# Optimization experiments

Hardware: AMD Instinct MI355X
Metric: run time of the kernel (lower is better)

Reference implementation:

```python
import jax, jax.numpy as jnp
import numpy as np

GRID = 4
N = GRID * GRID  # 16 nodes
CIN = 16
HID = 64
HEADS = 4
OUT = 256
NEG_SLOPE = 0.2  # PyG GATConv default leaky relu slope
LN_EPS = 1e-5


def _adj_mask():
    # 4-connected grid adjacency + self loops (PyG GATConv add_self_loops=True)
    m = np.zeros((N, N), dtype=bool)
    for i in range(GRID):
        for j in range(GRID):
            u = i * GRID + j
            if j + 1 < GRID:
                v = i * GRID + j + 1
                m[u, v] = m[v, u] = True
            if i + 1 < GRID:
                v = (i + 1) * GRID + j
                m[u, v] = m[v, u] = True
    np.fill_diagonal(m, True)
    return m

ADJ = jnp.asarray(_adj_mask())  # [N, N], adj[i, j] = j is a (self-)neighbor of i


def gat_layer(h, W, a_src, a_dst, b, concat):
    """PyG GATConv on the fixed grid graph, dense-masked form.
    h: [B, N, Fin]; W: [Fin, HEADS*C]; a_src/a_dst: [HEADS, C]."""
    B = h.shape[0]
    H, C = a_src.shape
    wh = (h @ W).reshape(B, N, H, C)                       # [B, N, H, C]
    e_src = jnp.einsum('bnhc,hc->bnh', wh, a_src)          # alpha_src . Wh_j
    e_dst = jnp.einsum('bnhc,hc->bnh', wh, a_dst)          # alpha_dst . Wh_i
    # score[b, i, j, h]: target i attends to source j
    e = e_dst[:, :, None, :] + e_src[:, None, :, :]
    e = jax.nn.leaky_relu(e, NEG_SLOPE)
    e = jnp.where(ADJ[None, :, :, None], e, -1e9)
    alpha = jax.nn.softmax(e, axis=2)                      # softmax over sources j
    out = jnp.einsum('bijh,bjhc->bihc', alpha, wh)         # [B, N, H, C]
    if concat:
        out = out.reshape(B, N, H * C)
    else:
        out = out.mean(axis=2)
    return out + b


def setup_inputs() -> dict:
    key = jax.random.key(0)
    ks = jax.random.split(key, 24)
    s = 0.05
    B = 16384
    inp = {
        'x': jax.random.normal(ks[0], (B, CIN, GRID, GRID), dtype=jnp.float32),
        'w_in': jax.random.normal(ks[1], (CIN, HID), dtype=jnp.float32) * s,
        'b_in': jnp.zeros((HID,), jnp.float32),
        # GAT layer 0: in 64 -> 4 heads x 64, concat
        'W0': jax.random.normal(ks[2], (HID, HEADS * HID), dtype=jnp.float32) * s,
        'asrc0': jax.random.normal(ks[3], (HEADS, HID), dtype=jnp.float32) * s,
        'adst0': jax.random.normal(ks[4], (HEADS, HID), dtype=jnp.float32) * s,
        'bb0': jnp.zeros((HEADS * HID,), jnp.float32),
        # GAT layer 1: in 256 -> 4 heads x 64, concat
        'W1': jax.random.normal(ks[5], (HEADS * HID, HEADS * HID), dtype=jnp.float32) * s,
        'asrc1': jax.random.normal(ks[6], (HEADS, HID), dtype=jnp.float32) * s,
        'adst1': jax.random.normal(ks[7], (HEADS, HID), dtype=jnp.float32) * s,
        'bb1': jnp.zeros((HEADS * HID,), jnp.float32),
        # GAT layer 2: in 256 -> 4 heads x 64, mean over heads (concat=False)
        'W2': jax.random.normal(ks[8], (HEADS * HID, HEADS * HID), dtype=jnp.float32) * s,
        'asrc2': jax.random.normal(ks[9], (HEADS, HID), dtype=jnp.float32) * s,
        'adst2': jax.random.normal(ks[10], (HEADS, HID), dtype=jnp.float32) * s,
        'bb2': jnp.zeros((HID,), jnp.float32),
        # output MLP: 64 -> 128 (LN, ReLU) -> 256
        'w1': jax.random.normal(ks[11], (HID, OUT // 2), dtype=jnp.float32) * s,
        'b1': jnp.zeros((OUT // 2,), jnp.float32),
        'ln_g': jnp.ones((OUT // 2,), jnp.float32),
        'ln_b': jnp.zeros((OUT // 2,), jnp.float32),
        'w2': jax.random.normal(ks[12], (OUT // 2, OUT), dtype=jnp.float32) * s,
        'b2': jnp.zeros((OUT,), jnp.float32),
    }
    return inp


def reference(x, w_in, b_in, W0, asrc0, adst0, bb0, W1, asrc1, adst1, bb1,
              W2, asrc2, adst2, bb2, w1, b1, ln_g, ln_b, w2, b2):
    B = x.shape[0]
    # grid_to_graph: (B, C, H, W) -> (B, N, C) node features
    h = jnp.transpose(x, (0, 2, 3, 1)).reshape(B, N, CIN)
    h = jax.nn.relu(h @ w_in + b_in)
    h = gat_layer(h, W0, asrc0, adst0, bb0, concat=True)
    h = jax.nn.relu(h)  # dropout is identity at inference
    h = gat_layer(h, W1, asrc1, adst1, bb1, concat=True)
    h = jax.nn.relu(h)
    h = gat_layer(h, W2, asrc2, adst2, bb2, concat=False)  # [B, N, 64]
    g = h.mean(axis=1)  # global_mean_pool over the 16 nodes of each graph
    # MLP with LayerNorm
    y = g @ w1 + b1
    mu = y.mean(axis=-1, keepdims=True)
    var = ((y - mu) ** 2).mean(axis=-1, keepdims=True)
    y = (y - mu) * jax.lax.rsqrt(var + LN_EPS) * ln_g + ln_b
    y = jax.nn.relu(y)
    return y @ w2 + b2
```

## Files before the change

### kernel.cpp

```cpp
#include <hip/hip_runtime.h>
#include <hip/hip_bf16.h>

typedef short s8v __attribute__((ext_vector_type(8)));
typedef short s4v __attribute__((ext_vector_type(4)));
typedef float f4v __attribute__((ext_vector_type(4)));

#define WSTR 36
#define AP   20
#define HIXBASE(s, quad) (((s)*4 + (quad))*256)

__device__ constexpr unsigned KMASK[16] = {
  0x0013u,0x0027u,0x004Eu,0x008Cu,
  0x0131u,0x0272u,0x04E4u,0x08C8u,
  0x1310u,0x2720u,0x4E40u,0x8C80u,
  0x3100u,0x7200u,0xE400u,0xC800u};

__device__ __forceinline__ short f2b(float x){
  __hip_bfloat16 h = __float2bfloat16(x);
  return *reinterpret_cast<short*>(&h);
}
__device__ __forceinline__ float b2f(short s){
  __hip_bfloat16 h = *reinterpret_cast<__hip_bfloat16*>(&s);
  return __bfloat162float(h);
}
__device__ __forceinline__ unsigned pk2(float a, float b){
  unsigned ua = __float_as_uint(a), ub = __float_as_uint(b);
  ua += 0x7fffu + ((ua >> 16) & 1u);
  ub += 0x7fffu + ((ub >> 16) & 1u);
  return __builtin_amdgcn_perm(ub, ua, 0x07060302);
}

__global__ __launch_bounds__(256) void prep_all(
  const float* __restrict__ W0, const float* __restrict__ as0, const float* __restrict__ ad0,
  const float* __restrict__ W1, const float* __restrict__ as1, const float* __restrict__ ad1,
  const float* __restrict__ W2, const float* __restrict__ as2, const float* __restrict__ ad2,
  const float* __restrict__ w_in,
  short* __restrict__ ws)
{
  short* WPin = ws;
  short* WP0  = ws + 2048;
  short* WP1  = ws + 2048 + 17408;
  short* WP2  = ws + 2048 + 17408 + 69632;

  const int t = threadIdx.x, l = t & 63;
  const int gid = blockIdx.x*4 + (t >> 6);

  if (gid < 288){
    const float* W; short* WP; int u = gid, f, s, KS;
    if (u < 32)      { W = W0; WP = WP0; KS = 2; f = u >> 1; s = u & 1; }
    else if (u < 160){ u -= 32;  W = W1; WP = WP1; KS = 8; f = u >> 3; s = u & 7; }
    else             { u -= 160; W = W2; WP = WP2; KS = 8; f = u >> 3; s = u & 7; }
    const int lq = l & 15, quad = l >> 4;
    union { s8v v; short s16[8]; } o;
    #pragma unroll
    for (int j = 0; j < 8; ++j)
      o.s16[j] = f2b(W[(s*32 + quad*8 + j)*256 + f*16 + lq]);
    *(s8v*)(WP + ((f*KS + s)*64 + l)*8) = o.v;
  } else if (gid < 292){
    const int f = gid - 288;
    const int lq = l & 15, quad = l >> 4;
    union { s8v v; short s16[8]; } o;
    #pragma unroll
    for (int j = 0; j < 8; ++j){
      const int k = quad*8 + j;
      o.s16[j] = (k < 16) ? f2b(w_in[k*64 + f*16 + lq]) : (short)0;
    }
    *(s8v*)(WPin + (f*64 + l)*8) = o.v;
  } else {
    int u = gid - 292;
    const float* W; const float* as; const float* ad; short* WP; int KS, k;
    if (u < 64)      { W=W0; as=as0; ad=ad0; WP=WP0; KS=2; k=u; }
    else if (u < 320){ u-=64;  W=W1; as=as1; ad=ad1; WP=WP1; KS=8; k=u; }
    else             { u-=320; W=W2; as=as2; ad=ad2; WP=WP2; KS=8; k=u; }
    float v[8];
    #pragma unroll
    for (int h = 0; h < 4; ++h){
      const float wv_ = W[k*256 + h*64 + l];
      v[h]   = wv_ * as[h*64 + l];
      v[4+h] = wv_ * ad[h*64 + l];
    }
    #pragma unroll
    for (int s = 1; s < 64; s <<= 1)
      #pragma unroll
      for (int uu = 0; uu < 8; ++uu) v[uu] += __shfl_xor(v[uu], s, 64);
    if (l < 16){
      const float r = (l < 8) ? v[l] : 0.f;
      WP[((16*KS + (k >> 5))*64 + ((k >> 3) & 3)*16 + l)*8 + (k & 7)] = f2b(r);
    }
  }
}

template<int KS, bool MEAN>
__device__ __forceinline__ void gat_layer(short* bufH, short* whT, short* alphaS,
    const short* __restrict__ WP, const float* __restrict__ bbias,
    float* __restrict__ out, const int b, const int t)
{
  const int l = t & 63, wv = t >> 6, lq = l & 15, quad = l >> 4;
  {
    f4v acc[5][2];
    #pragma unroll
    for (int fi = 0; fi < 5; ++fi)
      #pragma unroll
      for (int nt = 0; nt < 2; ++nt) acc[fi][nt] = (f4v){0.f,0.f,0.f,0.f};
    #pragma unroll
    for (int s = 0; s < KS; ++s){
      const s8v a0 = *(const s8v*)&bufH[HIXBASE(s, quad) + lq*8];
      const s8v a1 = *(const s8v*)&bufH[HIXBASE(s, quad) + (16 + lq)*8];
      #pragma unroll
      for (int fi = 0; fi < 5; ++fi){
        if (fi == 4 && wv != 3) break;
        const int f = (fi == 4) ? 16 : fi*4 + wv;
        const s8v bF = *(const s8v*)&WP[((f*KS + s)*64 + l)*8];
        acc[fi][0] = __builtin_amdgcn_mfma_f32_16x16x32_bf16(a0, bF, acc[fi][0], 0,0,0);
        acc[fi][1] = __builtin_amdgcn_mfma_f32_16x16x32_bf16(a1, bF, acc[fi][1], 0,0,0);
      }
    }
    #pragma unroll
    for (int fi = 0; fi < 5; ++fi){
      if (fi == 4 && (wv != 3 || lq >= 8)) break;
      const int f = (fi == 4) ? 16 : fi*4 + wv;
      #pragma unroll
      for (int nt = 0; nt < 2; ++nt){
        uint2 p;
        p.x = pk2(acc[fi][nt][0], acc[fi][nt][1]);
        p.y = pk2(acc[fi][nt][2], acc[fi][nt][3]);
        *(uint2*)&whT[(f*16 + lq)*WSTR + nt*16 + quad*4] = p;
      }
    }
  }
  __syncthreads();
  if (t < 128){
    const int g = t >> 6, h = (t >> 4) & 3, i = t & 15;
    const float ed = b2f(whT[(260 + h)*WSTR + g*16 + i]);
    float ev[16];
    #pragma unroll
    for (int c = 0; c < 4; ++c){
      const s4v v = *(const s4v*)&whT[(256 + h)*WSTR + g*16 + c*4];
      ev[c*4+0]=b2f(v[0]); ev[c*4+1]=b2f(v[1]); ev[c*4+2]=b2f(v[2]); ev[c*4+3]=b2f(v[3]);
    }
    const unsigned m = KMASK[i];
    float ssum = 0.f;
    #pragma unroll
    for (int j = 0; j < 16; ++j){
      float e = ed + ev[j];
      e = (e > 0.f) ? e : 0.2f*e;
      const float a = ((m >> j) & 1u) ? __expf(e) : 0.f;
      ev[j] = a; ssum += a;
    }
    const float inv = 1.f / ssum;
    unsigned* row = (unsigned*)&alphaS[((g*4 + h)*16 + i)*AP];
    #pragma unroll
    for (int c = 0; c < 8; ++c)
      row[c] = pk2(ev[2*c]*inv, ev[2*c+1]*inv);
  }
  __syncthreads();
  if constexpr (!MEAN){
    const int h = wv;
    union { s8v v; unsigned u[4]; } B[2];
    #pragma unroll
    for (int g = 0; g < 2; ++g){
      const unsigned* ar = (const unsigned*)&alphaS[((g*4 + h)*16 + lq)*AP + (quad & 1)*8];
      const bool act = ((quad >> 1) == g);
      #pragma unroll
      for (int c = 0; c < 4; ++c) B[g].u[c] = act ? ar[c] : 0u;
    }
    #pragma unroll
    for (int ct = 0; ct < 4; ++ct){
      const s8v a = *(const s8v*)&whT[(h*64 + ct*16 + lq)*WSTR + quad*8];
      const int sf = h*2 + (ct >> 1);
      const int qf = (ct & 1)*2 + (quad >> 1);
      const int jf = (quad & 1)*4;
      const int f0 = h*64 + ct*16 + quad*4;
      const float4 bb = *(const float4*)&bbias[f0];
      #pragma unroll
      for (int g = 0; g < 2; ++g){
        f4v d = (f4v){0.f,0.f,0.f,0.f};
        d = __builtin_amdgcn_mfma_f32_16x16x32_bf16(a, B[g].v, d, 0,0,0);
        uint2 p;
        p.x = pk2(fmaxf(d[0] + bb.x, 0.f), fmaxf(d[1] + bb.y, 0.f));
        p.y = pk2(fmaxf(d[2] + bb.z, 0.f), fmaxf(d[3] + bb.w, 0.f));
        *(uint2*)&bufH[HIXBASE(sf, qf) + (g*16 + lq)*8 + jf] = p;
      }
    }
  } else {
    const int g = wv >> 1;
    union { s8v v; unsigned u[4]; } B[4];
    #pragma unroll
    for (int h = 0; h < 4; ++h){
      const unsigned* ar = (const unsigned*)&alphaS[((g*4 + h)*16 + lq)*AP + (quad & 1)*8];
      const bool act = ((quad >> 1) == g);
      #pragma unroll
      for (int c = 0; c < 4; ++c) B[h].u[c] = act ? ar[c] : 0u;
    }
    #pragma unroll
    for (int cc = 0; cc < 2; ++cc){
      const int ct = (wv & 1)*2 + cc;
      f4v d = (f4v){0.f,0.f,0.f,0.f};
      #pragma unroll
      for (int h = 0; h < 4; ++h){
        const s8v a = *(const s8v*)&whT[(h*64 + ct*16 + lq)*WSTR + quad*8];
        d = __builtin_amdgcn_mfma_f32_16x16x32_bf16(a, B[h].v, d, 0,0,0);
      }
      #pragma unroll
      for (int s = 1; s < 16; s <<= 1){
        d[0] += __shfl_xor(d[0], s, 64); d[1] += __shfl_xor(d[1], s, 64);
        d[2] += __shfl_xor(d[2], s, 64); d[3] += __shfl_xor(d[3], s, 64);
      }
      if (lq == 0){
        const int f0 = ct*16 + quad*4;
        const float4 bb = *(const float4*)&bbias[f0];
        float4 gv;
        gv.x = d[0]*(1.f/64.f) + bb.x; gv.y = d[1]*(1.f/64.f) + bb.y;
        gv.z = d[2]*(1.f/64.f) + bb.z; gv.w = d[3]*(1.f/64.f) + bb.w;
        *(float4*)&out[((size_t)b*2 + g)*256 + f0] = gv;
      }
    }
  }
}

__global__ __launch_bounds__(256, 4) void gat_main(
  const float* __restrict__ x,
  const short* __restrict__ WPin, const float* __restrict__ b_in,
  const short* __restrict__ WP0,  const float* __restrict__ bb0,
  const short* __restrict__ WP1,  const float* __restrict__ bb1,
  const short* __restrict__ WP2,  const float* __restrict__ bb2,
  float* __restrict__ out)
{
  __shared__ __align__(16) short smem[8*4*32*8 + 264*WSTR + 8*16*AP];
  short* bufH   = smem;
  short* whT    = smem + 8192;
  short* alphaS = smem + 8192 + 264*WSTR;
  short* h0     = whT;
  constexpr int H0S = 40;

  const int b = blockIdx.x;
  const int t = threadIdx.x;
  const int l = t & 63, wv = t >> 6, lq = l & 15, quad = l >> 4;

  {
    const float2 v = *(const float2*)&x[b*512 + 2*t];
    const int i0 = 2*t;
    const int g = i0 >> 8, c = (i0 >> 4) & 15, n = i0 & 15;
    h0[(g*16 + n)*H0S + c]     = f2b(v.x);
    h0[(g*16 + n + 1)*H0S + c] = f2b(v.y);
    const int r = t >> 3, cc = 16 + 2*(t & 7);
    h0[r*H0S + cc] = 0; h0[r*H0S + cc + 1] = 0;
  }
  __syncthreads();

  {
    const s8v aF  = *(const s8v*)&WPin[(wv*64 + l)*8];
    const s8v b0v = *(const s8v*)&h0[lq*H0S + quad*8];
    const s8v b1v = *(const s8v*)&h0[(16+lq)*H0S + quad*8];
    f4v acc0 = (f4v){0.f,0.f,0.f,0.f}, acc1 = (f4v){0.f,0.f,0.f,0.f};
    acc0 = __builtin_amdgcn_mfma_f32_16x16x32_bf16(aF, b0v, acc0, 0,0,0);
    acc1 = __builtin_amdgcn_mfma_f32_16x16x32_bf16(aF, b1v, acc1, 0,0,0);
    const int f0 = wv*16 + quad*4;
    const float4 bi = *(const float4*)&b_in[f0];
    const int sf = wv >> 1;
    const int qf = (wv & 1)*2 + (quad >> 1);
    const int jf = (quad & 1)*4;
    uint2 p0, p1;
    p0.x = pk2(fmaxf(acc0[0]+bi.x,0.f), fmaxf(acc0[1]+bi.y,0.f));
    p0.y = pk2(fmaxf(acc0[2]+bi.z,0.f), fmaxf(acc0[3]+bi.w,0.f));
    p1.x = pk2(fmaxf(acc1[0]+bi.x,0.f), fmaxf(acc1[1]+bi.y,0.f));
    p1.y = pk2(fmaxf(acc1[2]+bi.z,0.f), fmaxf(acc1[3]+bi.w,0.f));
    *(uint2*)&bufH[HIXBASE(sf, qf) + lq*8 + jf]        = p0;
    *(uint2*)&bufH[HIXBASE(sf, qf) + (16 + lq)*8 + jf] = p1;
  }
  __syncthreads();

  gat_layer<2, false>(bufH, whT, alphaS, WP0, bb0, out, b, t);
  __syncthreads();
  gat_layer<8, false>(bufH, whT, alphaS, WP1, bb1, out, b, t);
  __syncthreads();
  gat_layer<8, true >(bufH, whT, alphaS, WP2, bb2, out, b, t);
}

__global__ __launch_bounds__(256) void mlp_tail(
  const float* __restrict__ w1,  const float* __restrict__ b1,
  const float* __restrict__ lng, const float* __restrict__ lnb,
  const float* __restrict__ w2,  const float* __restrict__ b2,
  float* __restrict__ out)
{
  __shared__ __align__(16) float gbuf[32*64];
  __shared__ __align__(16) float yb[32*128];
  __shared__ float red[64];
  const int t = threadIdx.x;
  const size_t gbase = (size_t)blockIdx.x * 32;

  #pragma unroll
  for (int u = 0; u < 2; ++u){
    const int id = u*256 + t;
    const int gr = id >> 4, c4 = id & 15;
    const float4 v = *(const float4*)&out[(gbase + gr)*256 + c4*4];
    *(float4*)&gbuf[gr*64 + c4*4] = v;
  }
  __syncthreads();

  const int o = t & 127, gs = t >> 7;
  float w1c[64];
  #pragma unroll
  for (int k = 0; k < 64; ++k) w1c[k] = w1[k*128 + o];
  const float b1v = b1[o];
  float y[16];
  #pragma unroll
  for (int i = 0; i < 16; ++i){
    const int gr = gs*16 + i;
    float acc = b1v;
    #pragma unroll
    for (int k4 = 0; k4 < 16; ++k4){
      const float4 gv = *(const float4*)&gbuf[gr*64 + k4*4];
      acc += gv.x*w1c[k4*4] + gv.y*w1c[k4*4+1] + gv.z*w1c[k4*4+2] + gv.w*w1c[k4*4+3];
    }
    y[i] = acc;
    yb[gr*128 + o] = acc;
  }
  __syncthreads();

  {
    const int gr = t >> 3, s = t & 7;
    float s1 = 0.f, s2 = 0.f;
    #pragma unroll
    for (int c4 = 0; c4 < 4; ++c4){
      const float4 v = *(const float4*)&yb[gr*128 + s*16 + c4*4];
      s1 += v.x + v.y + v.z + v.w;
      s2 += v.x*v.x + v.y*v.y + v.z*v.z + v.w*v.w;
    }
    #pragma unroll
    for (int d = 1; d < 8; d <<= 1){
      s1 += __shfl_xor(s1, d, 64);
      s2 += __shfl_xor(s2, d, 64);
    }
    if (s == 0){
      const float mu  = s1 * (1.f/128.f);
      const float var = s2 * (1.f/128.f) - mu*mu;
      red[gr*2]     = mu;
      red[gr*2 + 1] = rsqrtf(var + 1e-5f);
    }
  }
  __syncthreads();

  {
    const float lg = lng[o], lb = lnb[o];
    #pragma unroll
    for (int i = 0; i < 16; ++i){
      const int gr = gs*16 + i;
      const float yn = (y[i] - red[gr*2]) * red[gr*2 + 1] * lg + lb;
      yb[gr*128 + o] = fmaxf(yn, 0.f);
    }
  }
  __syncthreads();

  {
    const float b2v = b2[t];
    #pragma unroll
    for (int gh = 0; gh < 2; ++gh){
      float acc[16];
      #pragma unroll
      for (int g = 0; g < 16; ++g) acc[g] = b2v;
      #pragma unroll
      for (int kh = 0; kh < 2; ++kh){
        float w2c[64];
        #pragma unroll
        for (int k = 0; k < 64; ++k) w2c[k] = w2[(kh*64 + k)*256 + t];
        #pragma unroll
        for (int k4 = 0; k4 < 16; ++k4){
          #pragma unroll
          for (int g = 0; g < 16; ++g){
            const float4 yv = *(const float4*)&yb[(gh*16 + g)*128 + kh*64 + k4*4];
            acc[g] += yv.x*w2c[k4*4] + yv.y*w2c[k4*4+1] + yv.z*w2c[k4*4+2] + yv.w*w2c[k4*4+3];
          }
        }
      }
      #pragma unroll
      for (int g = 0; g < 16; ++g)
        out[(gbase + gh*16 + g)*256 + t] = acc[g];
    }
  }
}

extern "C" void kernel_launch(void* const* d_in, const int* in_sizes, int n_in,
                              void* d_out, int out_size, void* d_ws, size_t ws_size,
                              hipStream_t stream){
  const float* x    = (const float*)d_in[0];
  const float* w_in = (const float*)d_in[1];
  const float* b_in = (const float*)d_in[2];
  const float* W0   = (const float*)d_in[3];
  const float* as0  = (const float*)d_in[4];
  const float* ad0  = (const float*)d_in[5];
  const float* bb0  = (const float*)d_in[6];
  const float* W1   = (const float*)d_in[7];
  const float* as1  = (const float*)d_in[8];
  const float* ad1  = (const float*)d_in[9];
  const float* bb1  = (const float*)d_in[10];
  const float* W2   = (const float*)d_in[11];
  const float* as2  = (const float*)d_in[12];
  const float* ad2  = (const float*)d_in[13];
  const float* bb2  = (const float*)d_in[14];
  const float* w1   = (const float*)d_in[15];
  const float* b1   = (const float*)d_in[16];
  const float* lng  = (const float*)d_in[17];
  const float* lnb  = (const float*)d_in[18];
  const float* w2   = (const float*)d_in[19];
  const float* b2   = (const float*)d_in[20];
  const int B = in_sizes[0] / 256;

  short* ws = (short*)d_ws;
  const short* WPin = ws;
  const short* WP0  = ws + 2048;
  const short* WP1  = ws + 2048 + 17408;
  const short* WP2  = ws + 2048 + 17408 + 69632;

  prep_all<<<217, 256, 0, stream>>>(W0, as0, ad0, W1, as1, ad1, W2, as2, ad2,
                                    w_in, ws);
  gat_main<<<B/2, 256, 0, stream>>>(x, WPin, b_in, WP0, bb0, WP1, bb1, WP2, bb2,
                                    (float*)d_out);
  mlp_tail<<<B/32, 256, 0, stream>>>(w1, b1, lng, lnb, w2, b2, (float*)d_out);
}
```

Measured before the change: 324.8 us.

## Run the MLP tail GEMMs on bf16 MFMA with prepacked weight fragments

Adds a small prep kernel that converts w1 and w2 to bf16 and packs them into MFMA B-fragment order in the workspace. The MLP tail now stages pooled features and the post-LayerNorm activations as bf16 A-fragments in shared memory, and runs both linear layers with 16x16x32 bf16 MFMA instead of scalar fp32 FMA loops over register-cached weight columns. The aim is to cut the FMA-bound cost and register pressure of the tail. It adds an extra launch and bf16 rounding of the MLP inputs and weights. It also reuses workspace that overlaps the WP1 region, which stays safe only because the tail runs after gat_main in stream order.

```diff
diff --git a/kernel.cpp b/kernel.cpp
--- a/kernel.cpp
+++ b/kernel.cpp
@@ -277,105 +277,156 @@
   gat_layer<8, true >(bufH, whT, alphaS, WP2, bb2, out, b, t);
 }
 
+__global__ __launch_bounds__(256) void prep_tail(
+  const float* __restrict__ w1, const float* __restrict__ w2, short* __restrict__ ws)
+{
+  short* w1p = ws + 19456;
+  short* w2p = ws + 19456 + 8192;
+  const int t = threadIdx.x, l = t & 63;
+  const int task = blockIdx.x*4 + (t >> 6);
+  const int lq = l & 15, quad = l >> 4;
+  union { s8v v; short s16[8]; } o;
+  if (task < 16){
+    const int nt = task >> 1, s = task & 1;
+    #pragma unroll
+    for (int j = 0; j < 8; ++j)
+      o.s16[j] = f2b(w1[(s*32 + quad*8 + j)*128 + nt*16 + lq]);
+    *(s8v*)(w1p + (task*64 + l)*8) = o.v;
+  } else {
+    const int u = task - 16;
+    const int nt = u >> 2, s = u & 3;
+    #pragma unroll
+    for (int j = 0; j < 8; ++j)
+      o.s16[j] = f2b(w2[(s*32 + quad*8 + j)*256 + nt*16 + lq]);
+    *(s8v*)(w2p + (u*64 + l)*8) = o.v;
+  }
+}
+
 __global__ __launch_bounds__(256) void mlp_tail(
-  const float* __restrict__ w1,  const float* __restrict__ b1,
+  const short* __restrict__ w1p, const float* __restrict__ b1,
   const float* __restrict__ lng, const float* __restrict__ lnb,
-  const float* __restrict__ w2,  const float* __restrict__ b2,
+  const short* __restrict__ w2p, const float* __restrict__ b2,
   float* __restrict__ out)
 {
-  __shared__ __align__(16) float gbuf[32*64];
-  __shared__ __align__(16) float yb[32*128];
+  __shared__ __align__(16) short gAF[8*32*8];
+  __shared__ __align__(16) short yAF[16*32*8];
+  __shared__ __align__(16) float yF[32*132];
   __shared__ float red[64];
-  const int t = threadIdx.x;
+  const int t = threadIdx.x, l = t & 63, wv = t >> 6, lq = l & 15, quad = l >> 4;
   const size_t gbase = (size_t)blockIdx.x * 32;
 
-  #pragma unroll
-  for (int u = 0; u < 2; ++u){
-    const int id = u*256 + t;
-    const int gr = id >> 4, c4 = id & 15;
-    const float4 v = *(const float4*)&out[(gbase + gr)*256 + c4*4];
-    *(float4*)&gbuf[gr*64 + c4*4] = v;
-  }
-  __syncthreads();
-
-  const int o = t & 127, gs = t >> 7;
-  float w1c[64];
-  #pragma unroll
-  for (int k = 0; k < 64; ++k) w1c[k] = w1[k*128 + o];
-  const float b1v = b1[o];
-  float y[16];
-  #pragma unroll
-  for (int i = 0; i < 16; ++i){
-    const int gr = gs*16 + i;
-    float acc = b1v;
-    #pragma unroll
-    for (int k4 = 0; k4 < 16; ++k4){
-      const float4 gv = *(const float4*)&gbuf[gr*64 + k4*4];
-      acc += gv.x*w1c[k4*4] + gv.y*w1c[k4*4+1] + gv.z*w1c[k4*4+2] + gv.w*w1c[k4*4+3];
-    }
-    y[i] = acc;
-    yb[gr*128 + o] = acc;
-  }
-  __syncthreads();
-
-  {
-    const int gr = t >> 3, s = t & 7;
+  {
+    const int gr = t >> 3, grp = t & 7;
+    const float* gp = &out[(gbase + gr)*256 + grp*8];
+    const float4 v0 = *(const float4*)gp;
+    const float4 v1 = *(const float4*)(gp + 4);
+    uint4 p;
+    p.x = pk2(v0.x, v0.y); p.y = pk2(v0.z, v0.w);
+    p.z = pk2(v1.x, v1.y); p.w = pk2(v1.z, v1.w);
+    *(uint4*)&gAF[(grp*32 + gr)*8] = p;
+  }
+  __syncthreads();
+
+  {
+    f4v acc[2][2];
+    #pragma unroll
+    for (int mt = 0; mt < 2; ++mt)
+      #pragma unroll
+      for (int ntl = 0; ntl < 2; ++ntl) acc[mt][ntl] = (f4v){0.f,0.f,0.f,0.f};
+    #pragma unroll
+    for (int s = 0; s < 2; ++s){
+      const s8v a0 = *(const s8v*)&gAF[((s*4 + quad)*32 + lq)*8];
+      const s8v a1 = *(const s8v*)&gAF[((s*4 + quad)*32 + 16 + lq)*8];
+      #pragma unroll
+      for (int ntl = 0; ntl < 2; ++ntl){
+        const int nt = wv*2 + ntl;
+        const s8v bv = *(const s8v*)&w1p[((nt*2 + s)*64 + l)*8];
+        acc[0][ntl] = __builtin_amdgcn_mfma_f32_16x16x32_bf16(a0, bv, acc[0][ntl], 0,0,0);
+        acc[1][ntl] = __builtin_amdgcn_mfma_f32_16x16x32_bf16(a1, bv, acc[1][ntl], 0,0,0);
+      }
+    }
+    #pragma unroll
+    for (int ntl = 0; ntl < 2; ++ntl){
+      const int n = (wv*2 + ntl)*16 + lq;
+      const float bv = b1[n];
+      #pragma unroll
+      for (int mt = 0; mt < 2; ++mt)
+        #pragma unroll
+        for (int r = 0; r < 4; ++r)
+          yF[(mt*16 + quad*4 + r)*132 + n] = acc[mt][ntl][r] + bv;
+    }
+  }
+  __syncthreads();
+
+  {
+    const int m = t >> 3, s = t & 7;
     float s1 = 0.f, s2 = 0.f;
     #pragma unroll
     for (int c4 = 0; c4 < 4; ++c4){
-      const float4 v = *(const float4*)&yb[gr*128 + s*16 + c4*4];
+      const float4 v = *(const float4*)&yF[m*132 + s*16 + c4*4];
       s1 += v.x + v.y + v.z + v.w;
       s2 += v.x*v.x + v.y*v.y + v.z*v.z + v.w*v.w;
     }
     #pragma unroll
-    for (int d = 1; d < 8; d <<= 1){
-      s1 += __shfl_xor(s1, d, 64);
-      s2 += __shfl_xor(s2, d, 64);
-    }
+    for (int d = 1; d < 8; d <<= 1){ s1 += __shfl_xor(s1, d, 64); s2 += __shfl_xor(s2, d, 64); }
     if (s == 0){
       const float mu  = s1 * (1.f/128.f);
       const float var = s2 * (1.f/128.f) - mu*mu;
-      red[gr*2]     = mu;
-      red[gr*2 + 1] = rsqrtf(var + 1e-5f);
-    }
-  }
-  __syncthreads();
-
-  {
-    const float lg = lng[o], lb = lnb[o];
-    #pragma unroll
-    for (int i = 0; i < 16; ++i){
-      const int gr = gs*16 + i;
-      const float yn = (y[i] - red[gr*2]) * red[gr*2 + 1] * lg + lb;
-      yb[gr*128 + o] = fmaxf(yn, 0.f);
-    }
-  }
-  __syncthreads();
-
-  {
-    const float b2v = b2[t];
-    #pragma unroll
-    for (int gh = 0; gh < 2; ++gh){
-      float acc[16];
-      #pragma unroll
-      for (int g = 0; g < 16; ++g) acc[g] = b2v;
-      #pragma unroll
-      for (int kh = 0; kh < 2; ++kh){
-        float w2c[64];
+      red[m*2]     = mu;
+      red[m*2 + 1] = rsqrtf(var + 1e-5f);
+    }
+  }
+  __syncthreads();
+
+  {
+    const int m = t >> 3, s = t & 7;
+    const float mu = red[m*2], rs = red[m*2 + 1];
+    uint4 pa, pb;
+    float v[16];
+    #pragma unroll
+    for (int c4 = 0; c4 < 4; ++c4){
+      const float4 yv = *(const float4*)&yF[m*132 + s*16 + c4*4];
+      const float4 lg = *(const float4*)&lng[s*16 + c4*4];
+      const float4 lb = *(const float4*)&lnb[s*16 + c4*4];
+      v[c4*4+0] = fmaxf((yv.x - mu)*rs*lg.x + lb.x, 0.f);
+      v[c4*4+1] = fmaxf((yv.y - mu)*rs*lg.y + lb.y, 0.f);
+      v[c4*4+2] = fmaxf((yv.z - mu)*rs*lg.z + lb.z, 0.f);
+      v[c4*4+3] = fmaxf((yv.w - mu)*rs*lg.w + lb.w, 0.f);
+    }
+    pa.x = pk2(v[0],v[1]);  pa.y = pk2(v[2],v[3]);  pa.z = pk2(v[4],v[5]);  pa.w = pk2(v[6],v[7]);
+    pb.x = pk2(v[8],v[9]);  pb.y = pk2(v[10],v[11]); pb.z = pk2(v[12],v[13]); pb.w = pk2(v[14],v[15]);
+    *(uint4*)&yAF[((s*2    )*32 + m)*8] = pa;
+    *(uint4*)&yAF[((s*2 + 1)*32 + m)*8] = pb;
+  }
+  __syncthreads();
+
+  {
+    f4v acc[2][4];
+    #pragma unroll
+    for (int mt = 0; mt < 2; ++mt)
+      #pragma unroll
+      for (int ntl = 0; ntl < 4; ++ntl) acc[mt][ntl] = (f4v){0.f,0.f,0.f,0.f};
+    #pragma unroll
+    for (int s = 0; s < 4; ++s){
+      const s8v a0 = *(const s8v*)&yAF[((s*4 + quad)*32 + lq)*8];
+      const s8v a1 = *(const s8v*)&yAF[((s*4 + quad)*32 + 16 + lq)*8];
+      #pragma unroll
+      for (int ntl = 0; ntl < 4; ++ntl){
+        const int nt = wv*4 + ntl;
+        const s8v bv = *(const s8v*)&w2p[((nt*4 + s)*64 + l)*8];
+        acc[0][ntl] = __builtin_amdgcn_mfma_f32_16x16x32_bf16(a0, bv, acc[0][ntl], 0,0,0);
+        acc[1][ntl] = __builtin_amdgcn_mfma_f32_16x16x32_bf16(a1, bv, acc[1][ntl], 0,0,0);
+      }
+    }
+    #pragma unroll
+    for (int ntl = 0; ntl < 4; ++ntl){
+      const int n = (wv*4 + ntl)*16 + lq;
+      const float bv = b2[n];
+      #pragma unroll
+      for (int mt = 0; mt < 2; ++mt)
         #pragma unroll
-        for (int k = 0; k < 64; ++k) w2c[k] = w2[(kh*64 + k)*256 + t];
-        #pragma unroll
-        for (int k4 = 0; k4 < 16; ++k4){
-          #pragma unroll
-          for (int g = 0; g < 16; ++g){
-            const float4 yv = *(const float4*)&yb[(gh*16 + g)*128 + kh*64 + k4*4];
-            acc[g] += yv.x*w2c[k4*4] + yv.y*w2c[k4*4+1] + yv.z*w2c[k4*4+2] + yv.w*w2c[k4*4+3];
-          }
-        }
-      }
-      #pragma unroll
-      for (int g = 0; g < 16; ++g)
-        out[(gbase + gh*16 + g)*256 + t] = acc[g];
+        for (int r = 0; r < 4; ++r)
+          out[(gbase + mt*16 + quad*4 + r)*256 + n] = acc[mt][ntl][r] + bv;
     }
   }
 }
@@ -411,10 +462,13 @@
   const short* WP0  = ws + 2048;
   const short* WP1  = ws + 2048 + 17408;
   const short* WP2  = ws + 2048 + 17408 + 69632;
+  const short* w1p  = ws + 19456;
+  const short* w2p  = ws + 19456 + 8192;
 
   prep_all<<<217, 256, 0, stream>>>(W0, as0, ad0, W1, as1, ad1, W2, as2, ad2,
                                     w_in, ws);
   gat_main<<<B/2, 256, 0, stream>>>(x, WPin, b_in, WP0, bb0, WP1, bb1, WP2, bb2,
                                     (float*)d_out);
-  mlp_tail<<<B/32, 256, 0, stream>>>(w1, b1, lng, lnb, w2, b2, (float*)d_out);
-}
+  prep_tail<<<20, 256, 0, stream>>>(w1, w2, ws);
+  mlp_tail<<<B/32, 256, 0, stream>>>(w1p, b1, lng, lnb, w2p, b2, (float*)d_out);
+}
```

Result: faster. 287.4 us (-11.5%).
